# Optimization experiments

Measured on AMD Instinct MI355X. Metric: run time of the kernel, lower is better.

## Reference

```python
import jax, jax.numpy as jnp
import numpy as np

B, N, D, H, K = 8, 10000, 128, 4, 256
DH = D // H
M = N // 2


def make_pe(n, d):
    pos = jnp.arange(n, dtype=jnp.float32)[:, None]
    div = jnp.exp(jnp.arange(0, d, 2, dtype=jnp.float32) * (-jnp.log(10000.0) / d))
    ang = pos * div  # [n, d/2]
    pe = jnp.zeros((n, d), dtype=jnp.float32)
    pe = pe.at[:, 0::2].set(jnp.sin(ang))
    pe = pe.at[:, 1::2].set(jnp.cos(ang))
    return pe


def layernorm(z, g, b, eps=1e-5):
    mu = jnp.mean(z, -1, keepdims=True)
    var = jnp.var(z, -1, keepdims=True)
    return (z - mu) / jnp.sqrt(var + eps) * g + b


def setup_inputs():
    key = jax.random.key(0)
    ks = jax.random.split(key, 12)
    def rn(k, shape, scale):
        return jax.random.normal(k, shape, dtype=jnp.float32) * scale
    return {
        "x": rn(ks[0], (B, N), 1.0),
        "emb_w": rn(ks[1], (D, 1), 0.5),
        "emb_b": rn(ks[2], (D,), 0.02),
        "ln1_g": jnp.ones((D,), jnp.float32),
        "ln1_b": jnp.zeros((D,), jnp.float32),
        "wq": rn(ks[3], (D, D), D ** -0.5),
        "wk": rn(ks[4], (D, D), D ** -0.5),
        "wv": rn(ks[5], (D, D), D ** -0.5),
        "proj_k": rn(ks[6], (N, K), N ** -0.5),
        "proj_v": rn(ks[7], (N, K), N ** -0.5),
        "wo": rn(ks[8], (D, D), D ** -0.5),
        "wo_b": jnp.zeros((D,), jnp.float32),
        "ln2_g": jnp.ones((D,), jnp.float32),
        "ln2_b": jnp.zeros((D,), jnp.float32),
        "w1": rn(ks[9], (4 * D, D), D ** -0.5),
        "b1": jnp.zeros((4 * D,), jnp.float32),
        "w2": rn(ks[10], (D, 4 * D), (4 * D) ** -0.5),
        "b2": jnp.zeros((D,), jnp.float32),
        "fc_w": rn(ks[11], (M, N), N ** -0.5),
        "fc_b": jnp.zeros((M,), jnp.float32),
    }


def reference(x, emb_w, emb_b, ln1_g, ln1_b, wq, wk, wv, proj_k, proj_v, wo, wo_b,
              ln2_g, ln2_b, w1, b1, w2, b2, fc_w, fc_b):
    b, n = x.shape
    # Linear embedding of scalar per position: [B,N] -> [B,N,D]
    xe = x[..., None] @ emb_w.T + emb_b
    xe = xe + make_pe(n, D)
    # --- Linformer self-attention block (pre-norm + residual) ---
    hn = layernorm(xe, ln1_g, ln1_b)
    q = hn @ wq.T                                        # [B,N,D]
    k = jnp.einsum('bnd,nk->bkd', hn @ wk.T, proj_k)     # low-rank keys   [B,K,D]
    v = jnp.einsum('bnd,nk->bkd', hn @ wv.T, proj_v)     # low-rank values [B,K,D]
    q = q.reshape(b, n, H, DH).transpose(0, 2, 1, 3)     # [B,H,N,DH]
    k = k.reshape(b, K, H, DH).transpose(0, 2, 1, 3)     # [B,H,K,DH]
    v = v.reshape(b, K, H, DH).transpose(0, 2, 1, 3)
    attn = jax.nn.softmax(jnp.einsum('bhnd,bhkd->bhnk', q, k) * (DH ** -0.5), axis=-1)
    out = jnp.einsum('bhnk,bhkd->bhnd', attn, v).transpose(0, 2, 1, 3).reshape(b, n, D)
    xe = xe + out @ wo.T + wo_b
    # --- FeedForward block (pre-norm + residual, exact GELU) ---
    hn = layernorm(xe, ln2_g, ln2_b)
    xe = xe + (jax.nn.gelu(hn @ w1.T + b1, approximate=False) @ w2.T + b2)
    # fc over seq dim (Linear(N, N//2) applied to [B,D,N]) then sum-pool over D
    y = jnp.einsum('bnd,mn->bdm', xe, fc_w) + fc_b       # [B,D,M]
    return jnp.sum(y, axis=1)                            # [B,M]
```

## Files before the change

kernel.cpp:

```cpp
#include <hip/hip_runtime.h>

constexpr int B_ = 8, N_ = 10000, D_ = 128, H_ = 4, K_ = 256, M_ = 5000, DFF_ = 512;
constexpr int NPAD = 10240;

typedef __attribute__((ext_vector_type(8))) short bf16x8;
typedef __attribute__((ext_vector_type(4))) float f32x4;

__device__ __forceinline__ float bf2f(unsigned short u) {
    unsigned x = ((unsigned)u) << 16; float f; __builtin_memcpy(&f, &x, 4); return f;
}
__device__ __forceinline__ unsigned short f2bf(float f) {
    unsigned x; __builtin_memcpy(&x, &f, 4);
    x = (x + 0x7fffu + ((x >> 16) & 1u)) >> 16;
    return (unsigned short)x;
}
__device__ __forceinline__ unsigned pack2(float a, float b) {
    return (unsigned)f2bf(a) | ((unsigned)f2bf(b) << 16);
}
__device__ __forceinline__ float gelu_tanh(float v) {
    const float z = 0.7978845608028654f * fmaf(0.044715f * v, v * v, v);
    const float e = __expf(2.f * z);
    const float th = fmaf(-2.f, __builtin_amdgcn_rcpf(1.f + e), 1.f);
    return 0.5f * v * (1.f + th);
}

__global__ __launch_bounds__(256) void prep_k(
    const float* __restrict__ wq, const float* __restrict__ wk, const float* __restrict__ wv,
    const float* __restrict__ wo, const float* __restrict__ w1, const float* __restrict__ w2,
    unsigned short* __restrict__ wqb, unsigned short* __restrict__ wkb, unsigned short* __restrict__ wvb,
    unsigned short* __restrict__ wob, unsigned short* __restrict__ w1b, unsigned short* __restrict__ w2b,
    const float* __restrict__ pK, const float* __restrict__ pV, unsigned short* __restrict__ Pt)
{
    __shared__ __align__(16) char lds[16384];
    const int t = threadIdx.x;
    const int flat = blockIdx.x;

    if (flat < 192) {
        const int by = flat / 32, bx = flat % 32;
        const float* s; unsigned short* d; int sz;
        switch (by) {
            case 0: s = wq; d = wqb; sz = 16384; break;
            case 1: s = wk; d = wkb; sz = 16384; break;
            case 2: s = wv; d = wvb; sz = 16384; break;
            case 3: s = wo; d = wob; sz = 16384; break;
            case 4: s = w1; d = w1b; sz = 65536; break;
            default: s = w2; d = w2b; sz = 65536; break;
        }
        const int idx = (bx * 256 + t) * 8;
        if (idx >= sz) return;
        float4 a = *(const float4*)(s + idx);
        float4 b = *(const float4*)(s + idx + 4);
        uint4 p;
        p.x = pack2(a.x, a.y); p.y = pack2(a.z, a.w);
        p.z = pack2(b.x, b.y); p.w = pack2(b.z, b.w);
        *(uint4*)(d + idx) = p;
        return;
    }

    const int f = flat - 192;
    const int bx = f % 160, rest = f / 160;
    const int n0 = bx * 64, k0 = (rest & 1) * 128, which = rest >> 1;
    const float* P = which ? pV : pK;
    {
        const int nl = t >> 2, cc = t & 3;
        const int n = n0 + nl;
        uint4 v[4] = {};
        if (n < N_) {
            const float4* src = (const float4*)(P + (size_t)n * K_ + k0 + cc * 32);
            #pragma unroll
            for (int j = 0; j < 4; ++j) {
                float4 a = src[2 * j], b = src[2 * j + 1];
                uint4 p; p.x = pack2(a.x, a.y); p.y = pack2(a.z, a.w);
                p.z = pack2(b.x, b.y); p.w = pack2(b.z, b.w);
                v[j] = p;
            }
        }
        #pragma unroll
        for (int j = 0; j < 4; ++j) {
            int ch = (cc * 4 + j) ^ (nl & 15);
            *(uint4*)(lds + nl * 256 + ch * 16) = v[j];
        }
    }
    __syncthreads();
    {
        const int eb = t >> 3, nb = t & 7;
        unsigned short r0_[8], r1_[8], r2_[8], r3_[8];
        #pragma unroll
        for (int i = 0; i < 8; ++i) {
            int n = nb * 8 + i;
            int byte_ = n * 256 + (((eb >> 1) ^ (n & 15)) << 4) + ((eb & 1) << 3);
            uint2 dv = *(const uint2*)(lds + byte_);
            r0_[i] = (unsigned short)(dv.x & 0xffff); r1_[i] = (unsigned short)(dv.x >> 16);
            r2_[i] = (unsigned short)(dv.y & 0xffff); r3_[i] = (unsigned short)(dv.y >> 16);
        }
        size_t dbase = ((size_t)which * 256 + k0 + eb * 4) * NPAD + n0 + nb * 8;
        *(uint4*)&Pt[dbase]            = *(uint4*)r0_;
        *(uint4*)&Pt[dbase + NPAD]     = *(uint4*)r1_;
        *(uint4*)&Pt[dbase + 2 * NPAD] = *(uint4*)r2_;
        *(uint4*)&Pt[dbase + 3 * NPAD] = *(uint4*)r3_;
    }
}

__global__ __launch_bounds__(256) void hnt_k(
    const unsigned short* __restrict__ hn, unsigned short* __restrict__ hnT)
{
    __shared__ __align__(16) char lds[16384];
    const int t = threadIdx.x;
    const int n0 = blockIdx.x * 64, b = blockIdx.z;
    {
        const int nl = t >> 2, cc = t & 3;
        const int n = n0 + nl;
        uint4 v[4] = {};
        if (n < N_) {
            const uint4* src = (const uint4*)(hn + ((size_t)(b * N_ + n)) * D_ + cc * 32);
            #pragma unroll
            for (int j = 0; j < 4; ++j) v[j] = src[j];
        }
        #pragma unroll
        for (int j = 0; j < 4; ++j) {
            int ch = (cc * 4 + j) ^ (nl & 15);
            *(uint4*)(lds + nl * 256 + ch * 16) = v[j];
        }
    }
    __syncthreads();
    {
        const int eb = t >> 3, nb = t & 7;
        unsigned short r0_[8], r1_[8], r2_[8], r3_[8];
        #pragma unroll
        for (int i = 0; i < 8; ++i) {
            int n = nb * 8 + i;
            int byte_ = n * 256 + (((eb >> 1) ^ (n & 15)) << 4) + ((eb & 1) << 3);
            uint2 dv = *(const uint2*)(lds + byte_);
            r0_[i] = (unsigned short)(dv.x & 0xffff); r1_[i] = (unsigned short)(dv.x >> 16);
            r2_[i] = (unsigned short)(dv.y & 0xffff); r3_[i] = (unsigned short)(dv.y >> 16);
        }
        size_t dbase = ((size_t)b * 128 + eb * 4) * NPAD + n0 + nb * 8;
        *(uint4*)&hnT[dbase]            = *(uint4*)r0_;
        *(uint4*)&hnT[dbase + NPAD]     = *(uint4*)r1_;
        *(uint4*)&hnT[dbase + 2 * NPAD] = *(uint4*)r2_;
        *(uint4*)&hnT[dbase + 3 * NPAD] = *(uint4*)r3_;
    }
}

__global__ __launch_bounds__(256) void embed_ln_k(
    const float* __restrict__ x, const float* __restrict__ ew, const float* __restrict__ eb,
    const float* __restrict__ g, const float* __restrict__ bb,
    unsigned short* __restrict__ xeb, unsigned short* __restrict__ hnb)
{
    const int r = blockIdx.x * 4 + (threadIdx.x >> 6);
    const int lane = threadIdx.x & 63;
    const int n = r % N_;
    const float xv = x[r];
    const float ang = (float)n * expf((float)lane * -0.14391156829962788f);
    float sv, cv; sincosf(ang, &sv, &cv);
    const int d0 = 2 * lane;
    float e0 = xv * ew[d0]     + eb[d0]     + sv;
    float e1 = xv * ew[d0 + 1] + eb[d0 + 1] + cv;
    float sum = e0 + e1, sq = e0 * e0 + e1 * e1;
    #pragma unroll
    for (int off = 32; off; off >>= 1) { sum += __shfl_xor(sum, off); sq += __shfl_xor(sq, off); }
    const float mu = sum * (1.f / 128.f);
    const float var = sq * (1.f / 128.f) - mu * mu;
    const float rs = rsqrtf(var + 1e-5f);
    const size_t base = (size_t)r * D_ + d0;
    *(unsigned*)&xeb[base] = pack2(e0, e1);
    *(unsigned*)&hnb[base] = pack2((e0 - mu) * rs * g[d0] + bb[d0],
                                   (e1 - mu) * rs * g[d0 + 1] + bb[d0 + 1]);
}

enum { M_Q = 0, M_PROJ = 1, M_SMALL = 2, M_WO = 3 };

template<int MODE>
__global__ __launch_bounds__(256) void mgemm_k(
    const unsigned short* __restrict__ Abase, const unsigned short* __restrict__ Wbase,
    const unsigned short* __restrict__ Walt,
    const float* __restrict__ bias, float* __restrict__ Cf, unsigned short* __restrict__ Cb,
    const unsigned short* __restrict__ xebr, unsigned short* __restrict__ xebw,
    const float* __restrict__ lng, const float* __restrict__ lnb)
{
    constexpr int NSTEP = (MODE == M_PROJ) ? 20 : 4;
    constexpr int SA = (MODE == M_PROJ) ? NPAD : 128;
    constexpr int SB = SA;
    constexpr bool FUSED = (MODE == M_WO);

    __shared__ __align__(16) char lds[16384];

    const int t = threadIdx.x;
    const int bx = blockIdx.x, bz = blockIdx.z;

    const unsigned short* Ag; const unsigned short* Wg; size_t cbase;
    if (MODE == M_PROJ) {
        const int b = (bz >> 4) & 7, chunk = bz & 15, which = bz >> 7;
        Ag = Abase + (size_t)which * 256 * NPAD + (size_t)bx * 128 * NPAD + chunk * 640;
        Wg = Wbase + (size_t)b * 128 * NPAD + chunk * 640;
        cbase = (size_t)bz * 32768 + (size_t)bx * 16384;
    } else if (MODE == M_SMALL) {
        Ag = Abase + (size_t)bz * 2048 * 128 + (size_t)bx * 128 * 128;
        Wg = bz ? Walt : Wbase;
        cbase = (size_t)bz * 262144 + (size_t)bx * 16384;
    } else {
        Ag = Abase + (size_t)bx * 128 * SA;
        Wg = Wbase;
        cbase = (size_t)bx * 128 * 128;
    }

    const int srow = t >> 1, hib = 2 * (t & 1);
    const unsigned short* aptr = Ag + (size_t)srow * SA + hib * 8;
    const unsigned short* wptr = Wg + (size_t)srow * SB + hib * 8;
    const int swz = (srow >> 1) & 3;
    char* la0 = lds + srow * 64 + ((hib ^ swz) << 4);
    char* la1 = lds + srow * 64 + (((hib + 1) ^ swz) << 4);
    char* lw0 = la0 + 8192;
    char* lw1 = la1 + 8192;

    const int w = t >> 6, l = t & 63;
    const int g = l >> 4;
    const int wrow = (w & 1) * 64, wcol = (w >> 1) * 64;
    int offA[4], offW[4];
    #pragma unroll
    for (int mi = 0; mi < 4; ++mi) {
        int ra = wrow + mi * 16 + (l & 15);
        offA[mi] = ra * 64 + (((l >> 4) ^ ((ra >> 1) & 3)) << 4);
        int rw = wcol + mi * 16 + (l & 15);
        offW[mi] = 8192 + rw * 64 + (((l >> 4) ^ ((rw >> 1) & 3)) << 4);
    }

    f32x4 acc[4][4] = {};

    for (int s = 0; s < NSTEP; ++s) {
        uint4 va0 = *(const uint4*)(aptr);
        uint4 va1 = *(const uint4*)(aptr + 8);
        uint4 vw0 = *(const uint4*)(wptr);
        uint4 vw1 = *(const uint4*)(wptr + 8);
        aptr += 32; wptr += 32;
        __syncthreads();
        *(uint4*)la0 = va0; *(uint4*)la1 = va1;
        *(uint4*)lw0 = vw0; *(uint4*)lw1 = vw1;
        __syncthreads();
        bf16x8 af[4], bfr[4];
        #pragma unroll
        for (int mi = 0; mi < 4; ++mi) {
            af[mi] = *(const bf16x8*)(lds + offA[mi]);
            bfr[mi] = *(const bf16x8*)(lds + offW[mi]);
        }
        #pragma unroll
        for (int mi = 0; mi < 4; ++mi)
            #pragma unroll
            for (int ni = 0; ni < 4; ++ni)
                acc[mi][ni] = __builtin_amdgcn_mfma_f32_16x16x32_bf16(af[mi], bfr[ni], acc[mi][ni], 0, 0, 0);
    }

    const int lrb = wrow + (g << 2);
    const int lcb = wcol + (l & 15);

    if (FUSED) {
        float rsum[4][4], rsq[4][4];
        #pragma unroll
        for (int mi = 0; mi < 4; ++mi)
            #pragma unroll
            for (int r = 0; r < 4; ++r) { rsum[mi][r] = 0.f; rsq[mi][r] = 0.f; }
        #pragma unroll
        for (int mi = 0; mi < 4; ++mi)
            #pragma unroll
            for (int ni = 0; ni < 4; ++ni) {
                const int lc = lcb + ni * 16;
                #pragma unroll
                for (int r = 0; r < 4; ++r) {
                    const int lr = lrb + mi * 16 + r;
                    const size_t ci = cbase + (size_t)lr * 128 + lc;
                    float v = acc[mi][ni][r] + bias[lc] + bf2f(xebr[ci]);
                    acc[mi][ni][r] = v;
                    rsum[mi][r] += v;
                    rsq[mi][r] += v * v;
                }
            }
        #pragma unroll
        for (int mi = 0; mi < 4; ++mi)
            #pragma unroll
            for (int r = 0; r < 4; ++r) {
                float s_ = rsum[mi][r], q_ = rsq[mi][r];
                #pragma unroll
                for (int off = 1; off < 16; off <<= 1) {
                    s_ += __shfl_xor(s_, off);
                    q_ += __shfl_xor(q_, off);
                }
                rsum[mi][r] = s_; rsq[mi][r] = q_;
            }
        __syncthreads();
        float2* red = (float2*)lds;
        if ((l & 15) == 0) {
            #pragma unroll
            for (int mi = 0; mi < 4; ++mi)
                #pragma unroll
                for (int r = 0; r < 4; ++r) {
                    const int lr = lrb + mi * 16 + r;
                    float2 e; e.x = rsum[mi][r]; e.y = rsq[mi][r];
                    red[(w >> 1) * 128 + lr] = e;
                }
        }
        __syncthreads();
        #pragma unroll
        for (int mi = 0; mi < 4; ++mi)
            #pragma unroll
            for (int r = 0; r < 4; ++r) {
                const int lr = lrb + mi * 16 + r;
                const float2 e0 = red[lr], e1 = red[128 + lr];
                const float mu = (e0.x + e1.x) * (1.f / 128.f);
                const float var = (e0.y + e1.y) * (1.f / 128.f) - mu * mu;
                const float rstd = rsqrtf(var + 1e-5f);
                #pragma unroll
                for (int ni = 0; ni < 4; ++ni) {
                    const int lc = lcb + ni * 16;
                    const size_t ci = cbase + (size_t)lr * 128 + lc;
                    const float xv = acc[mi][ni][r];
                    xebw[ci] = f2bf(xv);
                    Cb[ci] = f2bf((xv - mu) * rstd * lng[lc] + lnb[lc]);
                }
            }
        return;
    }

    constexpr bool OBF = (MODE == M_Q || MODE == M_SMALL);
    #pragma unroll
    for (int mi = 0; mi < 4; ++mi) {
        #pragma unroll
        for (int ni = 0; ni < 4; ++ni) {
            const int lc = lcb + ni * 16;
            #pragma unroll
            for (int r = 0; r < 4; ++r) {
                const int lr = lrb + mi * 16 + r;
                const float v = acc[mi][ni][r];
                const size_t ci = cbase + (size_t)lr * 128 + lc;
                if (OBF) Cb[ci] = f2bf(v); else Cf[ci] = v;
            }
        }
    }
}

__global__ __launch_bounds__(256) void reduce_k(
    const float* __restrict__ partials, unsigned short* __restrict__ lowKV)
{
    const int gid = blockIdx.x * 256 + threadIdx.x;
    const int wb = gid >> 15, r = gid & 32767;
    const float* p = partials + (size_t)wb * 16 * 32768 + r;
    float s = 0.f;
    #pragma unroll
    for (int c = 0; c < 16; ++c) s += p[c * 32768];
    lowKV[gid] = f2bf(s);
}

__global__ __launch_bounds__(256) void ffn_k(
    const unsigned short* __restrict__ hnb, const unsigned short* __restrict__ w1b,
    const unsigned short* __restrict__ w2b, const float* __restrict__ b1,
    const float* __restrict__ b2, const unsigned short* __restrict__ xeb,
    float* __restrict__ st)
{
    __shared__ __align__(16) char lds[32768];
    const int t = threadIdx.x;
    const int w = t >> 6, l = t & 63;
    const int g = l >> 4, ql = l & 15;
    const int r0 = blockIdx.x * 64;
    const int wrow = (w & 1) * 32, wcol = (w >> 1) * 64;
    char* Ald = lds;
    char* Hld = lds + 16384;

    {
        const int rr = t >> 2, cc = t & 3;
        #pragma unroll
        for (int j = 0; j < 4; ++j) {
            const int ch = cc * 4 + j;
            const uint4 v = *(const uint4*)(hnb + (size_t)(r0 + rr) * 128 + ch * 8);
            *(uint4*)(Ald + rr * 256 + ((ch ^ (rr & 15)) << 4)) = v;
        }
    }
    __syncthreads();

    f32x4 acc[2][4] = {};
    #pragma unroll
    for (int hc = 0; hc < 4; ++hc) {
        f32x4 hacc[4][2] = {};
        #pragma unroll
        for (int ks = 0; ks < 4; ++ks) {
            const int e0 = ks * 32 + g * 8;
            bf16x8 hf[2], wf1[4];
            #pragma unroll
            for (int mi = 0; mi < 2; ++mi) {
                const int row = wrow + mi * 16 + ql;
                hf[mi] = *(const bf16x8*)(Ald + row * 256 + (((e0 >> 3) ^ (row & 15)) << 4));
            }
            #pragma unroll
            for (int ni = 0; ni < 4; ++ni) {
                const int c = hc * 128 + wcol + ni * 16 + ql;
                wf1[ni] = *(const bf16x8*)(w1b + (size_t)c * 128 + e0);
            }
            #pragma unroll
            for (int ni = 0; ni < 4; ++ni)
                #pragma unroll
                for (int mi = 0; mi < 2; ++mi)
                    hacc[ni][mi] = __builtin_amdgcn_mfma_f32_16x16x32_bf16(wf1[ni], hf[mi], hacc[ni][mi], 0, 0, 0);
        }
        #pragma unroll
        for (int ni = 0; ni < 4; ++ni) {
            const int colb = wcol + ni * 16 + g * 4;
            const float4 bb = *(const float4*)&b1[hc * 128 + colb];
            const int chunk = colb >> 3;
            const int sub = (colb & 4) << 1;
            #pragma unroll
            for (int mi = 0; mi < 2; ++mi) {
                const int row = wrow + mi * 16 + ql;
                uint2 pk;
                pk.x = pack2(gelu_tanh(hacc[ni][mi][0] + bb.x), gelu_tanh(hacc[ni][mi][1] + bb.y));
                pk.y = pack2(gelu_tanh(hacc[ni][mi][2] + bb.z), gelu_tanh(hacc[ni][mi][3] + bb.w));
                *(uint2*)(Hld + row * 256 + ((chunk ^ (row & 7)) << 4) + sub) = pk;
            }
        }
        __syncthreads();
        #pragma unroll
        for (int ks = 0; ks < 4; ++ks) {
            const int e0 = ks * 32 + g * 8;
            bf16x8 ah[2], wf2[4];
            #pragma unroll
            for (int mi = 0; mi < 2; ++mi) {
                const int row = wrow + mi * 16 + ql;
                ah[mi] = *(const bf16x8*)(Hld + row * 256 + (((e0 >> 3) ^ (row & 7)) << 4));
            }
            #pragma unroll
            for (int ni = 0; ni < 4; ++ni) {
                const int c = wcol + ni * 16 + ql;
                wf2[ni] = *(const bf16x8*)(w2b + (size_t)c * 512 + hc * 128 + e0);
            }
            #pragma unroll
            for (int mi = 0; mi < 2; ++mi)
                #pragma unroll
                for (int ni = 0; ni < 4; ++ni)
                    acc[mi][ni] = __builtin_amdgcn_mfma_f32_16x16x32_bf16(ah[mi], wf2[ni], acc[mi][ni], 0, 0, 0);
        }
        __syncthreads();
    }

    float rsum[2][4];
    #pragma unroll
    for (int mi = 0; mi < 2; ++mi)
        #pragma unroll
        for (int r = 0; r < 4; ++r) rsum[mi][r] = 0.f;
    #pragma unroll
    for (int mi = 0; mi < 2; ++mi)
        #pragma unroll
        for (int ni = 0; ni < 4; ++ni) {
            const int col = wcol + ni * 16 + ql;
            const float bias = b2[col];
            #pragma unroll
            for (int r = 0; r < 4; ++r) {
                const int row = wrow + mi * 16 + g * 4 + r;
                const size_t ci = (size_t)(r0 + row) * 128 + col;
                rsum[mi][r] += acc[mi][ni][r] + bias + bf2f(xeb[ci]);
            }
        }
    #pragma unroll
    for (int mi = 0; mi < 2; ++mi)
        #pragma unroll
        for (int r = 0; r < 4; ++r) {
            float s_ = rsum[mi][r];
            #pragma unroll
            for (int off = 1; off < 16; off <<= 1) s_ += __shfl_xor(s_, off);
            rsum[mi][r] = s_;
        }
    float* red = (float*)lds;
    if (ql == 0) {
        #pragma unroll
        for (int mi = 0; mi < 2; ++mi)
            #pragma unroll
            for (int r = 0; r < 4; ++r)
                red[(w >> 1) * 64 + wrow + mi * 16 + g * 4 + r] = rsum[mi][r];
    }
    __syncthreads();
    if (t < 64) {
        const float total = red[t] + red[64 + t];
        const int grow = r0 + t;
        const int bidx = grow / N_;
        const int n = grow - bidx * N_;
        st[(size_t)n * 8 + bidx] = total;
    }
}

__global__ __launch_bounds__(256) void attn_mfma_k(
    const unsigned short* __restrict__ q, const unsigned short* __restrict__ kv,
    unsigned short* __restrict__ outp)
{
    __shared__ __align__(16) char lds[65536];
    const int t = threadIdx.x;
    const int w = t >> 6, l = t & 63;
    const int g = l >> 4, ql = l & 15;
    const int h = blockIdx.y, b = blockIdx.z;
    const int q0 = blockIdx.x * 256;
    const float SC = 0.17677669529663687f;

    #pragma unroll
    for (int i = 0; i < 4; ++i) {
        const int r = (t >> 2) + 64 * i;
        const uint4 v = *(const uint4*)(kv + ((size_t)(b * 256 + r) * 128 + h * 32) + (t & 3) * 8);
        *(uint4*)(lds + r * 64 + (((t & 3) * 16) ^ ((r & 3) << 4))) = v;
    }
    {
        const int kp = t & 127, dhalf = t >> 7;
        const unsigned short* vsrc = kv + 262144 + ((size_t)(b * 256 + 2 * kp) * 128 + h * 32 + 16 * dhalf);
        uint4 a0 = *(const uint4*)(vsrc);
        uint4 a1 = *(const uint4*)(vsrc + 8);
        uint4 c0 = *(const uint4*)(vsrc + 128);
        uint4 c1 = *(const uint4*)(vsrc + 136);
        const unsigned short* pa0 = (const unsigned short*)&a0;
        const unsigned short* pa1 = (const unsigned short*)&a1;
        const unsigned short* pc0 = (const unsigned short*)&c0;
        const unsigned short* pc1 = (const unsigned short*)&c1;
        #pragma unroll
        for (int j = 0; j < 8; ++j) {
            const int row = 16 * dhalf + j;
            unsigned u = (unsigned)pa0[j] | ((unsigned)pc0[j] << 16);
            *(unsigned*)(lds + 16384 + row * 512 + ((4 * kp) ^ ((row & 7) << 4))) = u;
        }
        #pragma unroll
        for (int j = 0; j < 8; ++j) {
            const int row = 16 * dhalf + 8 + j;
            unsigned u = (unsigned)pa1[j] | ((unsigned)pc1[j] << 16);
            *(unsigned*)(lds + 16384 + row * 512 + ((4 * kp) ^ ((row & 7) << 4))) = u;
        }
    }
    bf16x8 qfr[4];
    #pragma unroll
    for (int qf = 0; qf < 4; ++qf) {
        int n = q0 + w * 64 + qf * 16 + ql;
        if (n >= N_) n = N_ - 1;
        qfr[qf] = *(const bf16x8*)(q + ((size_t)(b * N_ + n) * 128 + h * 32 + g * 8));
    }
    __syncthreads();

    char* Pw = lds + 32768 + w * 8192;
    f32x4 oacc[2][4] = {};
    float m_run[4], l_run[4];
    #pragma unroll
    for (int qf = 0; qf < 4; ++qf) { m_run[qf] = -1e30f; l_run[qf] = 0.f; }

    for (int kt = 0; kt < 4; ++kt) {
        const int kb = kt * 64;
        bf16x8 kfr[4];
        #pragma unroll
        for (int kf = 0; kf < 4; ++kf) {
            const int r = kb + kf * 16 + ql;
            kfr[kf] = *(const bf16x8*)(lds + r * 64 + ((g * 16) ^ ((r & 3) << 4)));
        }
        f32x4 s_[4][4];
        #pragma unroll
        for (int kf = 0; kf < 4; ++kf)
            #pragma unroll
            for (int qf = 0; qf < 4; ++qf) {
                f32x4 z = {0.f, 0.f, 0.f, 0.f};
                s_[kf][qf] = __builtin_amdgcn_mfma_f32_16x16x32_bf16(kfr[kf], qfr[qf], z, 0, 0, 0);
            }
        #pragma unroll
        for (int qf = 0; qf < 4; ++qf) {
            float mx = -1e30f;
            #pragma unroll
            for (int kf = 0; kf < 4; ++kf)
                #pragma unroll
                for (int r = 0; r < 4; ++r) mx = fmaxf(mx, s_[kf][qf][r]);
            mx = fmaxf(mx, __shfl_xor(mx, 16));
            mx = fmaxf(mx, __shfl_xor(mx, 32));
            mx *= SC;
            if (mx > m_run[qf]) {
                const float corr = __expf(m_run[qf] - mx);
                l_run[qf] *= corr;
                #pragma unroll
                for (int df = 0; df < 2; ++df) {
                    oacc[df][qf][0] *= corr; oacc[df][qf][1] *= corr;
                    oacc[df][qf][2] *= corr; oacc[df][qf][3] *= corr;
                }
                m_run[qf] = mx;
            }
            float p_[4][4]; float ssum = 0.f;
            #pragma unroll
            for (int kf = 0; kf < 4; ++kf)
                #pragma unroll
                for (int r = 0; r < 4; ++r) {
                    const float pv = __expf(s_[kf][qf][r] * SC - m_run[qf]);
                    p_[kf][r] = pv; ssum += pv;
                }
            ssum += __shfl_xor(ssum, 16);
            ssum += __shfl_xor(ssum, 32);
            l_run[qf] += ssum;
            const int qrow = qf * 16 + ql;
            #pragma unroll
            for (int kf = 0; kf < 4; ++kf) {
                uint2 pk;
                pk.x = pack2(p_[kf][0], p_[kf][1]);
                pk.y = pack2(p_[kf][2], p_[kf][3]);
                *(uint2*)(Pw + qrow * 128 + ((kf * 32 + g * 8) ^ ((qrow & 7) << 4))) = pk;
            }
        }
        asm volatile("s_waitcnt lgkmcnt(0)" ::: "memory");
        __builtin_amdgcn_sched_barrier(0);
        #pragma unroll
        for (int ks = 0; ks < 2; ++ks) {
            bf16x8 vt_[2];
            #pragma unroll
            for (int df = 0; df < 2; ++df) {
                const int row = df * 16 + ql;
                vt_[df] = *(const bf16x8*)(lds + 16384 + row * 512 +
                           ((kb * 2 + ks * 64 + g * 16) ^ ((row & 7) << 4)));
            }
            #pragma unroll
            for (int qf = 0; qf < 4; ++qf) {
                const int qrow = qf * 16 + ql;
                bf16x8 pf = *(const bf16x8*)(Pw + qrow * 128 + ((ks * 64 + g * 16) ^ ((qrow & 7) << 4)));
                #pragma unroll
                for (int df = 0; df < 2; ++df)
                    oacc[df][qf] = __builtin_amdgcn_mfma_f32_16x16x32_bf16(vt_[df], pf, oacc[df][qf], 0, 0, 0);
            }
        }
        asm volatile("s_waitcnt lgkmcnt(0)" ::: "memory");
        __builtin_amdgcn_sched_barrier(0);
    }

    float inv_[4];
    #pragma unroll
    for (int qf = 0; qf < 4; ++qf) inv_[4 - 4 + qf] = 1.f / l_run[qf];
    #pragma unroll
    for (int qf = 0; qf < 4; ++qf) {
        const int qrow = qf * 16 + ql;
        #pragma unroll
        for (int df = 0; df < 2; ++df) {
            const unsigned lo = pack2(oacc[df][qf][0] * inv_[qf], oacc[df][qf][1] * inv_[qf]);
            const unsigned hi = pack2(oacc[df][qf][2] * inv_[qf], oacc[df][qf][3] * inv_[qf]);
            *(unsigned*)(Pw + qrow * 64 + ((df * 32 + g * 8) ^ ((qrow & 3) << 4))) = lo;
            *(unsigned*)(Pw + qrow * 64 + ((df * 32 + g * 8 + 4) ^ ((qrow & 3) << 4))) = hi;
        }
    }
    asm volatile("s_waitcnt lgkmcnt(0)" ::: "memory");
    __builtin_amdgcn_sched_barrier(0);
    #pragma unroll
    for (int pp = 0; pp < 4; ++pp) {
        const int qrow = pp * 16 + (l >> 2), c = l & 3;
        const uint4 v = *(const uint4*)(Pw + qrow * 64 + ((c * 16) ^ ((qrow & 3) << 4)));
        const int n = q0 + w * 64 + qrow;
        if (n < N_)
            *(uint4*)(outp + ((size_t)(b * N_ + n) * 128 + h * 32 + c * 8)) = v;
    }
}

__global__ __launch_bounds__(256) void fc2_k(
    const float* __restrict__ st, const float* __restrict__ fcw,
    float* __restrict__ part)
{
    __shared__ float s_lds[16000];
    const int t = threadIdx.x;
    const int m0 = blockIdx.x * 64;
    const int n0 = blockIdx.y * 2000;

    const float4* src = (const float4*)(st + (size_t)n0 * 8);
    #pragma unroll 4
    for (int i = t; i < 4000; i += 256)
        ((float4*)s_lds)[i] = src[i];
    __syncthreads();

    const int mloc = t >> 2, q = t & 3;
    const int m = m0 + mloc;
    float acc[8] = {};
    if (m < M_) {
        const float* wrow = fcw + (size_t)m * N_ + n0;
        for (int k = 0; k < 125; ++k) {
            const int nn = q * 4 + k * 16;
            const float4 wv = *(const float4*)(wrow + nn);
            const float wl[4] = {wv.x, wv.y, wv.z, wv.w};
            #pragma unroll
            for (int j = 0; j < 4; ++j) {
                const float4 sa = *(const float4*)(s_lds + (nn + j) * 8);
                const float4 sb = *(const float4*)(s_lds + (nn + j) * 8 + 4);
                acc[0] = fmaf(wl[j], sa.x, acc[0]); acc[1] = fmaf(wl[j], sa.y, acc[1]);
                acc[2] = fmaf(wl[j], sa.z, acc[2]); acc[3] = fmaf(wl[j], sa.w, acc[3]);
                acc[4] = fmaf(wl[j], sb.x, acc[4]); acc[5] = fmaf(wl[j], sb.y, acc[5]);
                acc[6] = fmaf(wl[j], sb.z, acc[6]); acc[7] = fmaf(wl[j], sb.w, acc[7]);
            }
        }
    }
    #pragma unroll
    for (int j = 0; j < 8; ++j) {
        acc[j] += __shfl_xor(acc[j], 1);
        acc[j] += __shfl_xor(acc[j], 2);
    }
    if (q == 0 && m < M_) {
        float* pb = part + (size_t)blockIdx.y * 40000 + m;
        #pragma unroll
        for (int bb = 0; bb < 8; ++bb) pb[bb * 5000] = acc[bb];
    }
}

__global__ __launch_bounds__(256) void fc_combine_k(
    const float* __restrict__ part, const float* __restrict__ fcb,
    float* __restrict__ out)
{
    const int i = blockIdx.x * 256 + threadIdx.x;
    if (i >= 40000) return;
    float s = 0.f;
    #pragma unroll
    for (int c = 0; c < 5; ++c) s += part[c * 40000 + i];
    const int m = i % 5000;
    out[i] = s + 128.f * fcb[m];
}

extern "C" void kernel_launch(void* const* d_in, const int* in_sizes, int n_in,
                              void* d_out, int out_size, void* d_ws, size_t ws_size,
                              hipStream_t stream)
{
    const float* x      = (const float*)d_in[0];
    const float* emb_w  = (const float*)d_in[1];
    const float* emb_b  = (const float*)d_in[2];
    const float* ln1_g  = (const float*)d_in[3];
    const float* ln1_b  = (const float*)d_in[4];
    const float* wq     = (const float*)d_in[5];
    const float* wk     = (const float*)d_in[6];
    const float* wv     = (const float*)d_in[7];
    const float* projk  = (const float*)d_in[8];
    const float* projv  = (const float*)d_in[9];
    const float* wo     = (const float*)d_in[10];
    const float* wo_b   = (const float*)d_in[11];
    const float* ln2_g  = (const float*)d_in[12];
    const float* ln2_b  = (const float*)d_in[13];
    const float* w1     = (const float*)d_in[14];
    const float* b1     = (const float*)d_in[15];
    const float* w2     = (const float*)d_in[16];
    const float* b2     = (const float*)d_in[17];
    const float* fcw    = (const float*)d_in[18];
    const float* fcb    = (const float*)d_in[19];
    float* out = (float*)d_out;

    char* W = (char*)d_ws;
    unsigned short* xeb      = (unsigned short*)W;
    unsigned short* hnb      = (unsigned short*)(W + 40960000);
    char*           region   = W + 61440000;
    unsigned short* qb       = (unsigned short*)region;
    unsigned short* hnT      = (unsigned short*)(region + 20480000);
    unsigned short* Pt       = (unsigned short*)(region + 41451520);
    float*          partials = (float*)(region + 51937280);
    unsigned short* lowKV    = (unsigned short*)(W + 146931712);
    unsigned short* klowb    = (unsigned short*)(W + 147980288);
    unsigned short* wqb      = (unsigned short*)(W + 150077440);
    unsigned short* wkb      = wqb + 16384;
    unsigned short* wvb      = wkb + 16384;
    unsigned short* wob      = wvb + 16384;
    unsigned short* w1b      = wob + 16384;
    unsigned short* w2b      = w1b + 65536;
    float*          st       = (float*)(W + 150470656);
    float*          fcpart   = (float*)(W + 150790656);

    const size_t BN = (size_t)B_ * N_;

    prep_k<<<832, 256, 0, stream>>>(wq, wk, wv, wo, w1, w2, wqb, wkb, wvb, wob, w1b, w2b,
                                    projk, projv, Pt);
    embed_ln_k<<<BN / 4, 256, 0, stream>>>(x, emb_w, emb_b, ln1_g, ln1_b, xeb, hnb);
    hnt_k<<<dim3(160, 1, 8), 256, 0, stream>>>(hnb, hnT);
    mgemm_k<M_Q><<<dim3(625, 1, 1), 256, 0, stream>>>(hnb, wqb, nullptr, nullptr, nullptr, qb,
                                                      nullptr, nullptr, nullptr, nullptr);
    mgemm_k<M_PROJ><<<dim3(2, 1, 256), 256, 0, stream>>>(Pt, hnT, nullptr, nullptr, partials, nullptr,
                                                         nullptr, nullptr, nullptr, nullptr);
    reduce_k<<<2048, 256, 0, stream>>>(partials, lowKV);
    mgemm_k<M_SMALL><<<dim3(16, 1, 2), 256, 0, stream>>>(lowKV, wkb, wvb, nullptr, nullptr, klowb,
                                                         nullptr, nullptr, nullptr, nullptr);
    attn_mfma_k<<<dim3(40, H_, B_), 256, 0, stream>>>(qb, klowb, hnb);
    mgemm_k<M_WO><<<dim3(625, 1, 1), 256, 0, stream>>>(hnb, wob, nullptr, wo_b, nullptr, hnb,
                                                       xeb, xeb, ln2_g, ln2_b);
    ffn_k<<<1250, 256, 0, stream>>>(hnb, w1b, w2b, b1, b2, xeb, st);
    fc2_k<<<dim3(79, 5), 256, 0, stream>>>(st, fcw, fcpart);
    fc_combine_k<<<157, 256, 0, stream>>>(fcpart, fcb, out);
}
```

Baseline: 324.6 us.

## Fuse output projection and second layernorm into the FFN kernel

```diff
diff --git a/kernel.cpp b/kernel.cpp
--- a/kernel.cpp
+++ b/kernel.cpp
@@ -168,20 +168,17 @@
                                    (e1 - mu) * rs * g[d0 + 1] + bb[d0 + 1]);
 }
 
-enum { M_Q = 0, M_PROJ = 1, M_SMALL = 2, M_WO = 3 };
+enum { M_Q = 0, M_PROJ = 1, M_SMALL = 2 };
 
 template<int MODE>
 __global__ __launch_bounds__(256) void mgemm_k(
     const unsigned short* __restrict__ Abase, const unsigned short* __restrict__ Wbase,
     const unsigned short* __restrict__ Walt,
-    const float* __restrict__ bias, float* __restrict__ Cf, unsigned short* __restrict__ Cb,
-    const unsigned short* __restrict__ xebr, unsigned short* __restrict__ xebw,
-    const float* __restrict__ lng, const float* __restrict__ lnb)
+    float* __restrict__ Cf, unsigned short* __restrict__ Cb)
 {
     constexpr int NSTEP = (MODE == M_PROJ) ? 20 : 4;
     constexpr int SA = (MODE == M_PROJ) ? NPAD : 128;
     constexpr int SB = SA;
-    constexpr bool FUSED = (MODE == M_WO);
 
     __shared__ __align__(16) char lds[16384];
 
@@ -252,74 +249,6 @@
 
     const int lrb = wrow + (g << 2);
     const int lcb = wcol + (l & 15);
-
-    if (FUSED) {
-        float rsum[4][4], rsq[4][4];
-        #pragma unroll
-        for (int mi = 0; mi < 4; ++mi)
-            #pragma unroll
-            for (int r = 0; r < 4; ++r) { rsum[mi][r] = 0.f; rsq[mi][r] = 0.f; }
-        #pragma unroll
-        for (int mi = 0; mi < 4; ++mi)
-            #pragma unroll
-            for (int ni = 0; ni < 4; ++ni) {
-                const int lc = lcb + ni * 16;
-                #pragma unroll
-                for (int r = 0; r < 4; ++r) {
-                    const int lr = lrb + mi * 16 + r;
-                    const size_t ci = cbase + (size_t)lr * 128 + lc;
-                    float v = acc[mi][ni][r] + bias[lc] + bf2f(xebr[ci]);
-                    acc[mi][ni][r] = v;
-                    rsum[mi][r] += v;
-                    rsq[mi][r] += v * v;
-                }
-            }
-        #pragma unroll
-        for (int mi = 0; mi < 4; ++mi)
-            #pragma unroll
-            for (int r = 0; r < 4; ++r) {
-                float s_ = rsum[mi][r], q_ = rsq[mi][r];
-                #pragma unroll
-                for (int off = 1; off < 16; off <<= 1) {
-                    s_ += __shfl_xor(s_, off);
-                    q_ += __shfl_xor(q_, off);
-                }
-                rsum[mi][r] = s_; rsq[mi][r] = q_;
-            }
-        __syncthreads();
-        float2* red = (float2*)lds;
-        if ((l & 15) == 0) {
-            #pragma unroll
-            for (int mi = 0; mi < 4; ++mi)
-                #pragma unroll
-                for (int r = 0; r < 4; ++r) {
-                    const int lr = lrb + mi * 16 + r;
-                    float2 e; e.x = rsum[mi][r]; e.y = rsq[mi][r];
-                    red[(w >> 1) * 128 + lr] = e;
-                }
-        }
-        __syncthreads();
-        #pragma unroll
-        for (int mi = 0; mi < 4; ++mi)
-            #pragma unroll
-            for (int r = 0; r < 4; ++r) {
-                const int lr = lrb + mi * 16 + r;
-                const float2 e0 = red[lr], e1 = red[128 + lr];
-                const float mu = (e0.x + e1.x) * (1.f / 128.f);
-                const float var = (e0.y + e1.y) * (1.f / 128.f) - mu * mu;
-                const float rstd = rsqrtf(var + 1e-5f);
-                #pragma unroll
-                for (int ni = 0; ni < 4; ++ni) {
-                    const int lc = lcb + ni * 16;
-                    const size_t ci = cbase + (size_t)lr * 128 + lc;
-                    const float xv = acc[mi][ni][r];
-                    xebw[ci] = f2bf(xv);
-                    Cb[ci] = f2bf((xv - mu) * rstd * lng[lc] + lnb[lc]);
-                }
-            }
-        return;
-    }
-
     constexpr bool OBF = (MODE == M_Q || MODE == M_SMALL);
     #pragma unroll
     for (int mi = 0; mi < 4; ++mi) {
@@ -349,13 +278,15 @@
     lowKV[gid] = f2bf(s);
 }
 
-__global__ __launch_bounds__(256) void ffn_k(
-    const unsigned short* __restrict__ hnb, const unsigned short* __restrict__ w1b,
-    const unsigned short* __restrict__ w2b, const float* __restrict__ b1,
-    const float* __restrict__ b2, const unsigned short* __restrict__ xeb,
+__global__ __launch_bounds__(256) void wo_ffn_k(
+    const unsigned short* __restrict__ attn_out, const unsigned short* __restrict__ wob,
+    const float* __restrict__ wo_bias, const unsigned short* __restrict__ xeb,
+    const float* __restrict__ lng, const float* __restrict__ lnb,
+    const unsigned short* __restrict__ w1b, const float* __restrict__ b1,
+    const unsigned short* __restrict__ w2b, const float* __restrict__ b2,
     float* __restrict__ st)
 {
-    __shared__ __align__(16) char lds[32768];
+    __shared__ __align__(16) char lds[51200];
     const int t = threadIdx.x;
     const int w = t >> 6, l = t & 63;
     const int g = l >> 4, ql = l & 15;
@@ -363,19 +294,113 @@
     const int wrow = (w & 1) * 32, wcol = (w >> 1) * 64;
     char* Ald = lds;
     char* Hld = lds + 16384;
+    char* A2ld = lds + 32768;
+    float2* red  = (float2*)(lds + 49152);
+    float*  stp  = (float*) (lds + 50176);
+    float*  redF = (float*) (lds + 50432);
+
+    float wob_c[4], lng_c[4], lnb_c[4], b2_c[4];
+    #pragma unroll
+    for (int ni = 0; ni < 4; ++ni) {
+        const int col = wcol + ni * 16 + ql;
+        wob_c[ni] = wo_bias[col]; lng_c[ni] = lng[col];
+        lnb_c[ni] = lnb[col];     b2_c[ni] = b2[col];
+    }
 
     {
         const int rr = t >> 2, cc = t & 3;
         #pragma unroll
         for (int j = 0; j < 4; ++j) {
             const int ch = cc * 4 + j;
-            const uint4 v = *(const uint4*)(hnb + (size_t)(r0 + rr) * 128 + ch * 8);
+            const uint4 v = *(const uint4*)(attn_out + (size_t)(r0 + rr) * 128 + ch * 8);
             *(uint4*)(Ald + rr * 256 + ((ch ^ (rr & 15)) << 4)) = v;
         }
     }
     __syncthreads();
 
     f32x4 acc[2][4] = {};
+    #pragma unroll
+    for (int ks = 0; ks < 4; ++ks) {
+        const int e0 = ks * 32 + g * 8;
+        bf16x8 af[2], wf[4];
+        #pragma unroll
+        for (int mi = 0; mi < 2; ++mi) {
+            const int row = wrow + mi * 16 + ql;
+            af[mi] = *(const bf16x8*)(Ald + row * 256 + (((e0 >> 3) ^ (row & 15)) << 4));
+        }
+        #pragma unroll
+        for (int ni = 0; ni < 4; ++ni) {
+            const int c = wcol + ni * 16 + ql;
+            wf[ni] = *(const bf16x8*)(wob + (size_t)c * 128 + e0);
+        }
+        #pragma unroll
+        for (int mi = 0; mi < 2; ++mi)
+            #pragma unroll
+            for (int ni = 0; ni < 4; ++ni)
+                acc[mi][ni] = __builtin_amdgcn_mfma_f32_16x16x32_bf16(af[mi], wf[ni], acc[mi][ni], 0, 0, 0);
+    }
+
+    float rsum[2][4], rsq[2][4];
+    #pragma unroll
+    for (int mi = 0; mi < 2; ++mi)
+        #pragma unroll
+        for (int r = 0; r < 4; ++r) { rsum[mi][r] = 0.f; rsq[mi][r] = 0.f; }
+    #pragma unroll
+    for (int mi = 0; mi < 2; ++mi)
+        #pragma unroll
+        for (int ni = 0; ni < 4; ++ni) {
+            const int col = wcol + ni * 16 + ql;
+            #pragma unroll
+            for (int r = 0; r < 4; ++r) {
+                const int row = wrow + mi * 16 + g * 4 + r;
+                float v = acc[mi][ni][r] + wob_c[ni] + bf2f(xeb[(size_t)(r0 + row) * 128 + col]);
+                acc[mi][ni][r] = v;
+                rsum[mi][r] += v;
+                rsq[mi][r] += v * v;
+            }
+        }
+    #pragma unroll
+    for (int mi = 0; mi < 2; ++mi)
+        #pragma unroll
+        for (int r = 0; r < 4; ++r) {
+            float s_ = rsum[mi][r], q_ = rsq[mi][r];
+            #pragma unroll
+            for (int off = 1; off < 16; off <<= 1) { s_ += __shfl_xor(s_, off); q_ += __shfl_xor(q_, off); }
+            rsum[mi][r] = s_; rsq[mi][r] = q_;
+        }
+    if (ql == 0) {
+        #pragma unroll
+        for (int mi = 0; mi < 2; ++mi)
+            #pragma unroll
+            for (int r = 0; r < 4; ++r) {
+                const int row = wrow + mi * 16 + g * 4 + r;
+                float2 e; e.x = rsum[mi][r]; e.y = rsq[mi][r];
+                red[(w >> 1) * 64 + row] = e;
+            }
+    }
+    __syncthreads();
+
+    #pragma unroll
+    for (int mi = 0; mi < 2; ++mi)
+        #pragma unroll
+        for (int r = 0; r < 4; ++r) {
+            const int row = wrow + mi * 16 + g * 4 + r;
+            const float2 e0 = red[row], e1 = red[64 + row];
+            const float tot = e0.x + e1.x;
+            const float mu = tot * (1.f / 128.f);
+            const float var = (e0.y + e1.y) * (1.f / 128.f) - mu * mu;
+            const float rstd = rsqrtf(var + 1e-5f);
+            if (ql == 0 && w < 2) stp[row] = tot;
+            #pragma unroll
+            for (int ni = 0; ni < 4; ++ni) {
+                const int col = wcol + ni * 16 + ql;
+                const float hn2 = (acc[mi][ni][r] - mu) * rstd * lng_c[ni] + lnb_c[ni];
+                *(unsigned short*)(A2ld + row * 256 + (((col >> 3) ^ (row & 15)) << 4) + (col & 7) * 2) = f2bf(hn2);
+            }
+        }
+    __syncthreads();
+
+    f32x4 accF[2][4] = {};
     #pragma unroll
     for (int hc = 0; hc < 4; ++hc) {
         f32x4 hacc[4][2] = {};
@@ -386,7 +411,7 @@
             #pragma unroll
             for (int mi = 0; mi < 2; ++mi) {
                 const int row = wrow + mi * 16 + ql;
-                hf[mi] = *(const bf16x8*)(Ald + row * 256 + (((e0 >> 3) ^ (row & 15)) << 4));
+                hf[mi] = *(const bf16x8*)(A2ld + row * 256 + (((e0 >> 3) ^ (row & 15)) << 4));
             }
             #pragma unroll
             for (int ni = 0; ni < 4; ++ni) {
@@ -433,49 +458,42 @@
             for (int mi = 0; mi < 2; ++mi)
                 #pragma unroll
                 for (int ni = 0; ni < 4; ++ni)
-                    acc[mi][ni] = __builtin_amdgcn_mfma_f32_16x16x32_bf16(ah[mi], wf2[ni], acc[mi][ni], 0, 0, 0);
+                    accF[mi][ni] = __builtin_amdgcn_mfma_f32_16x16x32_bf16(ah[mi], wf2[ni], accF[mi][ni], 0, 0, 0);
         }
         __syncthreads();
     }
 
-    float rsum[2][4];
+    float rF[2][4];
     #pragma unroll
     for (int mi = 0; mi < 2; ++mi)
         #pragma unroll
-        for (int r = 0; r < 4; ++r) rsum[mi][r] = 0.f;
+        for (int r = 0; r < 4; ++r) rF[mi][r] = 0.f;
     #pragma unroll
     for (int mi = 0; mi < 2; ++mi)
         #pragma unroll
-        for (int ni = 0; ni < 4; ++ni) {
-            const int col = wcol + ni * 16 + ql;
-            const float bias = b2[col];
-            #pragma unroll
-            for (int r = 0; r < 4; ++r) {
-                const int row = wrow + mi * 16 + g * 4 + r;
-                const size_t ci = (size_t)(r0 + row) * 128 + col;
-                rsum[mi][r] += acc[mi][ni][r] + bias + bf2f(xeb[ci]);
-            }
-        }
+        for (int ni = 0; ni < 4; ++ni)
+            #pragma unroll
+            for (int r = 0; r < 4; ++r)
+                rF[mi][r] += accF[mi][ni][r] + b2_c[ni];
     #pragma unroll
     for (int mi = 0; mi < 2; ++mi)
         #pragma unroll
         for (int r = 0; r < 4; ++r) {
-            float s_ = rsum[mi][r];
+            float s_ = rF[mi][r];
             #pragma unroll
             for (int off = 1; off < 16; off <<= 1) s_ += __shfl_xor(s_, off);
-            rsum[mi][r] = s_;
-        }
-    float* red = (float*)lds;
+            rF[mi][r] = s_;
+        }
     if (ql == 0) {
         #pragma unroll
         for (int mi = 0; mi < 2; ++mi)
             #pragma unroll
             for (int r = 0; r < 4; ++r)
-                red[(w >> 1) * 64 + wrow + mi * 16 + g * 4 + r] = rsum[mi][r];
+                redF[(w >> 1) * 64 + wrow + mi * 16 + g * 4 + r] = rF[mi][r];
     }
     __syncthreads();
     if (t < 64) {
-        const float total = red[t] + red[64 + t];
+        const float total = redF[t] + redF[64 + t] + stp[t];
         const int grow = r0 + t;
         const int bidx = grow / N_;
         const int n = grow - bidx * N_;
@@ -622,7 +640,7 @@
 
     float inv_[4];
     #pragma unroll
-    for (int qf = 0; qf < 4; ++qf) inv_[4 - 4 + qf] = 1.f / l_run[qf];
+    for (int qf = 0; qf < 4; ++qf) inv_[qf] = 1.f / l_run[qf];
     #pragma unroll
     for (int qf = 0; qf < 4; ++qf) {
         const int qrow = qf * 16 + ql;
@@ -757,17 +775,12 @@
                                     projk, projv, Pt);
     embed_ln_k<<<BN / 4, 256, 0, stream>>>(x, emb_w, emb_b, ln1_g, ln1_b, xeb, hnb);
     hnt_k<<<dim3(160, 1, 8), 256, 0, stream>>>(hnb, hnT);
-    mgemm_k<M_Q><<<dim3(625, 1, 1), 256, 0, stream>>>(hnb, wqb, nullptr, nullptr, nullptr, qb,
-                                                      nullptr, nullptr, nullptr, nullptr);
-    mgemm_k<M_PROJ><<<dim3(2, 1, 256), 256, 0, stream>>>(Pt, hnT, nullptr, nullptr, partials, nullptr,
-                                                         nullptr, nullptr, nullptr, nullptr);
+    mgemm_k<M_Q><<<dim3(625, 1, 1), 256, 0, stream>>>(hnb, wqb, nullptr, nullptr, qb);
+    mgemm_k<M_PROJ><<<dim3(2, 1, 256), 256, 0, stream>>>(Pt, hnT, nullptr, partials, nullptr);
     reduce_k<<<2048, 256, 0, stream>>>(partials, lowKV);
-    mgemm_k<M_SMALL><<<dim3(16, 1, 2), 256, 0, stream>>>(lowKV, wkb, wvb, nullptr, nullptr, klowb,
-                                                         nullptr, nullptr, nullptr, nullptr);
+    mgemm_k<M_SMALL><<<dim3(16, 1, 2), 256, 0, stream>>>(lowKV, wkb, wvb, nullptr, klowb);
     attn_mfma_k<<<dim3(40, H_, B_), 256, 0, stream>>>(qb, klowb, hnb);
-    mgemm_k<M_WO><<<dim3(625, 1, 1), 256, 0, stream>>>(hnb, wob, nullptr, wo_b, nullptr, hnb,
-                                                       xeb, xeb, ln2_g, ln2_b);
-    ffn_k<<<1250, 256, 0, stream>>>(hnb, w1b, w2b, b1, b2, xeb, st);
+    wo_ffn_k<<<1250, 256, 0, stream>>>(hnb, wob, wo_b, xeb, ln2_g, ln2_b, w1b, b1, w2b, b2, st);
     fc2_k<<<dim3(79, 5), 256, 0, stream>>>(st, fcw, fcpart);
     fc_combine_k<<<157, 256, 0, stream>>>(fcpart, fcb, out);
 }
```

New measurement: 331.4 us. 2.1% more time.
